# Kernel tuning notes

Measured on AMD Instinct MI355X. Metric: run time of the kernel, lower is better.

The kernel has to match this reference:

```python
import jax, jax.numpy as jnp
import numpy as np

B, L, C, H = 4, 2048, 1024, 16
D = C // H            # head_dim = 64
TAU = 4
SCALE = 1.0 / np.sqrt(D) / TAU  # cos_attn=False path


def setup_inputs() -> dict:
    key = jax.random.key(0)
    ks = jax.random.split(key, 7)
    std = 1.0 / np.sqrt(C)
    return {
        "x": jax.random.normal(ks[0], (B, L, C), dtype=jnp.float32),
        "attn_bias": jax.random.normal(ks[1], (1, 1, L, L), dtype=jnp.float32) * 0.02,
        "W_qkv": jax.random.normal(ks[2], (3 * C, C), dtype=jnp.float32) * std,
        "q_bias": jax.random.normal(ks[3], (C,), dtype=jnp.float32) * 0.02,
        "v_bias": jax.random.normal(ks[4], (C,), dtype=jnp.float32) * 0.02,
        "W_proj": jax.random.normal(ks[5], (C, C), dtype=jnp.float32) * std,
        "b_proj": jax.random.normal(ks[6], (C,), dtype=jnp.float32) * 0.02,
    }


def reference(x, attn_bias, W_qkv, q_bias, v_bias, W_proj, b_proj):
    # qkv projection with bias = cat(q_bias, zeros_k, v_bias)
    bias = jnp.concatenate([q_bias, jnp.zeros_like(q_bias), v_bias])
    qkv = x @ W_qkv.T + bias                      # [B, L, 3C]
    qkv = qkv.reshape(B, L, 3, H, D)
    q, k, v = jnp.moveaxis(qkv, 2, 0)             # each [B, L, H, D]
    q = q.transpose(0, 2, 1, 3)                   # [B, H, L, D]
    k = k.transpose(0, 2, 1, 3)
    v = v.transpose(0, 2, 1, 3)
    # slow_attn: (q*scale) @ k^T + bias -> softmax -> @ v
    scores = jnp.einsum("bhqd,bhkd->bhqk", q * SCALE, k) + attn_bias
    attn = jax.nn.softmax(scores, axis=-1)
    oup = jnp.einsum("bhqk,bhkd->bhqd", attn, v)  # [B, H, L, D]
    oup = oup.transpose(0, 2, 1, 3).reshape(B, L, C)
    return oup @ W_proj.T + b_proj
```

## Files before the change

### kernel.cpp

```cpp
#include <hip/hip_runtime.h>
#include <hip/hip_bf16.h>

typedef unsigned short u16;
typedef unsigned int   u32;

using f32x4  = __attribute__((ext_vector_type(4)))  float;
using f32x16 = __attribute__((ext_vector_type(16))) float;
using s16x8  = __attribute__((ext_vector_type(8)))  short;
using b16x8  = __attribute__((ext_vector_type(8)))  __bf16;
using u32x4  = __attribute__((ext_vector_type(4)))  u32;

#define LOG2E 1.44269504088896f
#define QSC   (0.03125f * LOG2E)

__device__ __forceinline__ f32x4 mfma16(s16x8 a, s16x8 b, f32x4 c) {
  return __builtin_amdgcn_mfma_f32_16x16x32_bf16(
      __builtin_bit_cast(b16x8, a), __builtin_bit_cast(b16x8, b), c, 0, 0, 0);
}
__device__ __forceinline__ f32x16 mfma32(s16x8 a, s16x8 b, f32x16 c) {
  return __builtin_amdgcn_mfma_f32_32x32x16_bf16(
      __builtin_bit_cast(b16x8, a), __builtin_bit_cast(b16x8, b), c, 0, 0, 0);
}

__device__ __forceinline__ u16 f2bf(float f) {
  u32 u = __builtin_bit_cast(u32, f);
  u = (u + 0x7FFFu + ((u >> 16) & 1u)) >> 16;
  return (u16)u;
}
__device__ __forceinline__ float exp2_hw(float x) {
  float r;
  asm("v_exp_f32 %0, %1" : "=v"(r) : "v"(x));
  return r;
}
__device__ __forceinline__ u32 cvtpk(float a, float b) {
  u32 r;
  asm("v_cvt_pk_bf16_f32 %0, %1, %2" : "=v"(r) : "v"(a), "v"(b));
  return r;
}

__device__ __forceinline__ void gload16(const void* g, void* l) {
  __builtin_amdgcn_global_load_lds(
      (const __attribute__((address_space(1))) u32*)g,
      (__attribute__((address_space(3))) u32*)l, 16, 0, 0);
}

__global__ void cvt3(const float* __restrict__ x, const float* __restrict__ wqkv,
                     const float* __restrict__ wproj, u16* __restrict__ out) {
  int i = blockIdx.x * blockDim.x + threadIdx.x;
  const int stride = gridDim.x * blockDim.x;
  for (; i < 3145728; i += stride) {
    const float* src = (i < 2097152) ? x + 4 * (long)i
                     : (i < 2883584) ? wqkv + 4 * ((long)i - 2097152)
                                     : wproj + 4 * ((long)i - 2883584);
    const float4 v = *(const float4*)src;
    ushort4 o;
    o.x = f2bf(v.x); o.y = f2bf(v.y); o.z = f2bf(v.z); o.w = f2bf(v.w);
    ((ushort4*)out)[i] = o;
  }
}

__global__ void bias_rearrange(const float* __restrict__ ab, u16* __restrict__ out) {
  __shared__ u16 T[32][72];
  const int tid  = threadIdx.x;
  const int slot = blockIdx.x >> 5;
  const int kt   = blockIdx.x & 31;

  {
    const int qr = tid >> 3;
    const int fc = (tid & 7) * 8;
    const float* src = ab + (long)(slot * 32 + qr) * 2048 + kt * 64 + fc;
    const float4 a = *(const float4*)(src);
    const float4 b = *(const float4*)(src + 4);
    u16 t[8];
    t[0] = f2bf(a.x * LOG2E); t[1] = f2bf(a.y * LOG2E);
    t[2] = f2bf(a.z * LOG2E); t[3] = f2bf(a.w * LOG2E);
    t[4] = f2bf(b.x * LOG2E); t[5] = f2bf(b.y * LOG2E);
    t[6] = f2bf(b.z * LOG2E); t[7] = f2bf(b.w * LOG2E);
    *(s16x8*)&T[qr][fc] = *(s16x8*)t;
  }
  __syncthreads();

  {
    const int chunk = tid >> 6;
    const int lane  = tid & 63;
    const int q5    = lane & 31;
    const int hi    = lane >> 5;
    u16 o[8];
#pragma unroll
    for (int e = 0; e < 8; ++e) {
      const int vidx = chunk * 8 + e;
      const int kb = vidx >> 4, r = vidx & 15;
      const int key = kb * 32 + (r & 3) + 8 * (r >> 2) + 4 * hi;
      o[e] = T[q5][key];
    }
    *(s16x8*)(out + ((long)blockIdx.x * 256 + tid) * 8) = *(s16x8*)o;
  }
}

template<int EPI>
__global__ __launch_bounds__(256)
void gemm_bt(const u16* __restrict__ A, const u16* __restrict__ Bm,
             int M, int N, int K,
             const float* __restrict__ bias0, const float* __restrict__ bias1,
             u16* __restrict__ oq, u16* __restrict__ ok, u16* __restrict__ ov,
             float* __restrict__ outf)
{
  __shared__ u16 As[2][128 * 32];
  __shared__ u16 Bs[2][128 * 32];

  const int tid  = threadIdx.x;
  const int w    = tid >> 6;
  const int lane = tid & 63;
  const int lr   = lane & 15;
  const int lg   = lane >> 4;
  const int wr   = w >> 1, wc = w & 1;

  const int bm = blockIdx.y, bn = blockIdx.x;

  f32x4 acc[4][4];
#pragma unroll
  for (int i = 0; i < 4; ++i)
#pragma unroll
    for (int j = 0; j < 4; ++j) acc[i][j] = (f32x4){0.f, 0.f, 0.f, 0.f};

  const int rowA = bm * 128 + (tid >> 2);
  const int rowB = bn * 128 + (tid >> 2);
  const int colk = (tid & 3) * 8;

  const u16* ga0 = A  + (long)rowA * K + colk;
  const u16* gb0 = Bm + (long)rowB * K + colk;

  gload16(ga0,          &As[0][w * 512]);
  gload16(ga0 + 64 * K, &As[0][2048 + w * 512]);
  gload16(gb0,          &Bs[0][w * 512]);
  gload16(gb0 + 64 * K, &Bs[0][2048 + w * 512]);
  asm volatile("s_waitcnt vmcnt(0)" ::: "memory");
  __syncthreads();

  const int NT = K >> 5;
  for (int t = 0; t < NT; ++t) {
    const int cur = t & 1;
    if (t + 1 < NT) {
      const u16* ga = ga0 + (t + 1) * 32;
      const u16* gb = gb0 + (t + 1) * 32;
      gload16(ga,          &As[cur ^ 1][w * 512]);
      gload16(ga + 64 * K, &As[cur ^ 1][2048 + w * 512]);
      gload16(gb,          &Bs[cur ^ 1][w * 512]);
      gload16(gb + 64 * K, &Bs[cur ^ 1][2048 + w * 512]);
    }

    s16x8 af[4], bfr[4];
#pragma unroll
    for (int mi = 0; mi < 4; ++mi)
      af[mi] = *(const s16x8*)(&As[cur][(wr * 64 + mi * 16 + lr) * 32 + lg * 8]);
#pragma unroll
    for (int ni = 0; ni < 4; ++ni)
      bfr[ni] = *(const s16x8*)(&Bs[cur][(wc * 64 + ni * 16 + lr) * 32 + lg * 8]);
#pragma unroll
    for (int mi = 0; mi < 4; ++mi)
#pragma unroll
      for (int ni = 0; ni < 4; ++ni)
        acc[mi][ni] = mfma16(af[mi], bfr[ni], acc[mi][ni]);

    asm volatile("s_waitcnt vmcnt(0)" ::: "memory");
    __syncthreads();
  }

  const int gm0 = bm * 128 + wr * 64;
  const int gn0 = bn * 128 + wc * 64;

#pragma unroll
  for (int mi = 0; mi < 4; ++mi) {
#pragma unroll
    for (int ni = 0; ni < 4; ++ni) {
      const int col  = gn0 + ni * 16 + lr;
      const int row0 = gm0 + mi * 16 + lg * 4;
      if (EPI == 0) {
        const int which = col >> 10;
        const int cj    = col & 1023;
        const float badd = (which == 0) ? bias0[cj] : (which == 2 ? bias1[cj] : 0.f);
        const int h = cj >> 6, d = cj & 63;
#pragma unroll
        for (int r = 0; r < 4; ++r) {
          const int rowg = row0 + r;
          const int b = rowg >> 11, l = rowg & 2047;
          const int bh = b * 16 + h;
          float val = acc[mi][ni][r] + badd;
          if (which == 0) val *= QSC;
          const u16 o = f2bf(val);
          if (which == 0)      oq[(bh * 2048 + l) * 64 + d] = o;
          else if (which == 1) ok[(bh * 2048 + l) * 64 + d] = o;
          else {
            const int lp = (l & ~12) | ((l & 4) << 1) | ((l & 8) >> 1);
            ov[(bh * 64 + d) * 2048 + lp] = o;
          }
        }
      } else {
        const float badd = bias0[col];
#pragma unroll
        for (int r = 0; r < 4; ++r)
          outf[(long)(row0 + r) * N + col] = acc[mi][ni][r] + badd;
      }
    }
  }
}

__global__ __launch_bounds__(256)
void flash_attn(const u16* __restrict__ qbuf, const u16* __restrict__ kbuf,
                const u16* __restrict__ vtbuf, const u16* __restrict__ biasr,
                u16* __restrict__ oup)
{
  __shared__ u16 Ks[2][64 * 72];
  __shared__ u16 Vs[2][64 * 72];

  const int tid  = threadIdx.x;
  const int w    = tid >> 6;
  const int lane = tid & 63;
  const int lq   = lane & 31;
  const int hi   = lane >> 5;

  const int bid = blockIdx.x;
  const int swz = (bid & 7) * 128 + (bid >> 3);
  const int bh  = swz >> 4, qt2 = swz & 15;
  const long base = (long)bh * (2048 * 64);

  const int qrow = qt2 * 128 + w * 32 + lq;
  s16x8 qf[4];
  {
    const u16* qp = qbuf + base + qrow * 64 + 8 * hi;
#pragma unroll
    for (int s = 0; s < 4; ++s) qf[s] = *(const s16x8*)(qp + 16 * s);
  }

  f32x16 oacc0, oacc1;
  float lacc[8];
#pragma unroll
  for (int r = 0; r < 16; ++r) { oacc0[r] = 0.f; oacc1[r] = 0.f; }
#pragma unroll
  for (int r = 0; r < 8; ++r) lacc[r] = 0.f;

  const u16* bslice = biasr + (long)(qt2 * 4 + w) * 65536 + lane * 8;

  const int sr  = tid >> 3;
  const int scc = tid & 7;
  const u16* kg = kbuf  + base + sr * 64   + scc * 8;
  const u16* vg = vtbuf + base + sr * 2048 + scc * 8;
  const int wo0 = sr * 72 + scc * 8;
  const int wo1 = (32 + sr) * 72 + scc * 8;

  {
    const s16x8 a0 = *(const s16x8*)(kg);
    const s16x8 a1 = *(const s16x8*)(kg + 2048);
    const s16x8 b0 = *(const s16x8*)(vg);
    const s16x8 b1 = *(const s16x8*)(vg + 65536);
    *(s16x8*)(&Ks[0][wo0]) = a0;  *(s16x8*)(&Ks[0][wo1]) = a1;
    *(s16x8*)(&Vs[0][wo0]) = b0;  *(s16x8*)(&Vs[0][wo1]) = b1;
  }
  __syncthreads();

  for (int kt = 0; kt < 32; ++kt) {
    const int cur = kt & 1;

    s16x8 nk0, nk1, nv0, nv1;
    if (kt < 31) {
      const u16* kn = kg + (kt + 1) * 4096;
      const u16* vn = vg + (kt + 1) * 64;
      nk0 = *(const s16x8*)(kn);
      nk1 = *(const s16x8*)(kn + 2048);
      nv0 = *(const s16x8*)(vn);
      nv1 = *(const s16x8*)(vn + 65536);
    }

    s16x8 kf0[4], kf1[4], vf0[4], vf1[4];
    {
      const u16* kb0 = &Ks[cur][lq * 72];
      const u16* kb1 = &Ks[cur][(32 + lq) * 72];
      const u16* vb0 = &Vs[cur][lq * 72];
      const u16* vb1 = &Vs[cur][(32 + lq) * 72];
#pragma unroll
      for (int s = 0; s < 4; ++s) {
        const int off = (2 * s + hi) * 8;
        kf0[s] = *(const s16x8*)(kb0 + off);
        kf1[s] = *(const s16x8*)(kb1 + off);
        vf0[s] = *(const s16x8*)(vb0 + off);
        vf1[s] = *(const s16x8*)(vb1 + off);
      }
    }

    u32x4 bb[4];
#pragma unroll
    for (int k = 0; k < 4; ++k)
      bb[k] = *(const u32x4*)(bslice + kt * 2048 + k * 512);

    f32x16 sa0, sa1;
#pragma unroll
    for (int jw = 0; jw < 8; ++jw) {
      const u32 w0 = bb[jw >> 2][jw & 3];
      const u32 w1 = bb[2 + (jw >> 2)][jw & 3];
      sa0[2 * jw]     = __builtin_bit_cast(float, w0 << 16);
      sa0[2 * jw + 1] = __builtin_bit_cast(float, w0 & 0xFFFF0000u);
      sa1[2 * jw]     = __builtin_bit_cast(float, w1 << 16);
      sa1[2 * jw + 1] = __builtin_bit_cast(float, w1 & 0xFFFF0000u);
    }

#pragma unroll
    for (int s = 0; s < 4; ++s) sa0 = mfma32(kf0[s], qf[s], sa0);
#pragma unroll
    for (int s = 0; s < 4; ++s) sa1 = mfma32(kf1[s], qf[s], sa1);

#pragma unroll
    for (int r = 0; r < 16; ++r) {
      sa0[r] = exp2_hw(sa0[r]);
      sa1[r] = exp2_hw(sa1[r]);
    }
#pragma unroll
    for (int r = 0; r < 8; ++r)
      lacc[r] += (sa0[r] + sa0[r + 8]) + (sa1[r] + sa1[r + 8]);

    s16x8 pf[4];
#pragma unroll
    for (int ks = 0; ks < 4; ++ks) {
      const f32x16 ps = (ks & 2) ? sa1 : sa0;
      const int o = (ks & 1) * 8;
      u32x4 tt;
      tt[0] = cvtpk(ps[o + 0], ps[o + 1]);
      tt[1] = cvtpk(ps[o + 2], ps[o + 3]);
      tt[2] = cvtpk(ps[o + 4], ps[o + 5]);
      tt[3] = cvtpk(ps[o + 6], ps[o + 7]);
      pf[ks] = __builtin_bit_cast(s16x8, tt);
    }

#pragma unroll
    for (int ks = 0; ks < 4; ++ks) {
      oacc0 = mfma32(vf0[ks], pf[ks], oacc0);
      oacc1 = mfma32(vf1[ks], pf[ks], oacc1);
    }

    if (kt < 31) {
      *(s16x8*)(&Ks[cur ^ 1][wo0]) = nk0;
      *(s16x8*)(&Ks[cur ^ 1][wo1]) = nk1;
      *(s16x8*)(&Vs[cur ^ 1][wo0]) = nv0;
      *(s16x8*)(&Vs[cur ^ 1][wo1]) = nv1;
    }
    __syncthreads();
  }

  u32 (*Os)[32][33] = (u32(*)[32][33])&Ks[0][0];
  const int b = bh >> 4, h = bh & 15;
  float l = ((lacc[0] + lacc[1]) + (lacc[2] + lacc[3]))
          + ((lacc[4] + lacc[5]) + (lacc[6] + lacc[7]));
  l += __shfl_xor(l, 32, 64);
  const float inv = 1.f / l;
#pragma unroll
  for (int i = 0; i < 8; ++i) {
    const int idx = (i & 1) + 2 * hi + 4 * (i >> 1);
    Os[w][lq][idx]      = cvtpk(oacc0[2 * i] * inv, oacc0[2 * i + 1] * inv);
    Os[w][lq][idx + 16] = cvtpk(oacc1[2 * i] * inv, oacc1[2 * i + 1] * inv);
  }
  __syncthreads();
#pragma unroll
  for (int it = 0; it < 4; ++it) {
    const int q = it * 8 + (lane >> 3);
    const int c = (lane & 7) * 4;
    u32x4 v;
#pragma unroll
    for (int j = 0; j < 4; ++j) v[j] = Os[w][q][c + j];
    const long row = (long)(b * 2048 + qt2 * 128 + w * 32 + q);
    *(u32x4*)(oup + row * 1024 + h * 64 + (lane & 7) * 8) = v;
  }
}

extern "C" void kernel_launch(void* const* d_in, const int* in_sizes, int n_in,
                              void* d_out, int out_size, void* d_ws, size_t ws_size,
                              hipStream_t stream) {
  const float* x     = (const float*)d_in[0];
  const float* ab    = (const float*)d_in[1];
  const float* wqkv  = (const float*)d_in[2];
  const float* qbias = (const float*)d_in[3];
  const float* vbias = (const float*)d_in[4];
  const float* wproj = (const float*)d_in[5];
  const float* bproj = (const float*)d_in[6];
  float* out = (float*)d_out;

  char* ws = (char*)d_ws;
  if (ws_size < 83886080u) return;
  u16* xb     = (u16*)(ws);
  u16* wqkvb  = (u16*)(ws + 16777216);
  u16* wprojb = (u16*)(ws + 23068672);
  u16* biasr  = (u16*)(ws + 25165824);
  u16* qbuf   = (u16*)(ws + 33554432);
  u16* kbuf   = (u16*)(ws + 50331648);
  u16* vtbuf  = (u16*)(ws + 67108864);

  cvt3<<<dim3(2048), dim3(256), 0, stream>>>(x, wqkv, wproj, xb);
  bias_rearrange<<<dim3(2048), dim3(256), 0, stream>>>(ab, biasr);

  gemm_bt<0><<<dim3(24, 64), dim3(256), 0, stream>>>(
      xb, wqkvb, 8192, 3072, 1024, qbias, vbias, qbuf, kbuf, vtbuf, nullptr);

  flash_attn<<<dim3(1024), dim3(256), 0, stream>>>(qbuf, kbuf, vtbuf, biasr, xb);

  gemm_bt<1><<<dim3(8, 64), dim3(256), 0, stream>>>(
      xb, wprojb, 8192, 1024, 1024, bproj, nullptr, nullptr, nullptr, nullptr, out);
}
```

Measured before the change: 229.8 us.

## Triple-buffer GEMM shared-memory tiles with partial vmcnt waits

Moves the bf16 GEMM from double to triple buffering of the A/B shared tiles. Loads for tile t+2 are issued right after a single barrier per iteration, and a partial vmcnt wait lets the following tile's loads stay in flight while the current tile is computed. This removes one full vmcnt(0) drain and one barrier per k-step, in exchange for 50% more LDS per block, which may reduce occupancy. It relies on gload16 being a direct-to-LDS load counted by vmcnt, so that vmcnt(4) exactly matches the four loads of one stage.

```diff
diff --git a/kernel.cpp b/kernel.cpp
--- a/kernel.cpp
+++ b/kernel.cpp
@@ -105,8 +105,8 @@
              u16* __restrict__ oq, u16* __restrict__ ok, u16* __restrict__ ov,
              float* __restrict__ outf)
 {
-  __shared__ u16 As[2][128 * 32];
-  __shared__ u16 Bs[2][128 * 32];
+  __shared__ u16 As[3][128 * 32];
+  __shared__ u16 Bs[3][128 * 32];
 
   const int tid  = threadIdx.x;
   const int w    = tid >> 6;
@@ -130,24 +130,26 @@
   const u16* ga0 = A  + (long)rowA * K + colk;
   const u16* gb0 = Bm + (long)rowB * K + colk;
 
-  gload16(ga0,          &As[0][w * 512]);
-  gload16(ga0 + 64 * K, &As[0][2048 + w * 512]);
-  gload16(gb0,          &Bs[0][w * 512]);
-  gload16(gb0 + 64 * K, &Bs[0][2048 + w * 512]);
-  asm volatile("s_waitcnt vmcnt(0)" ::: "memory");
-  __syncthreads();
+#define GSTAGE(BUF, T)                                          \
+  {                                                             \
+    const u16* ga = ga0 + (T) * 32;                             \
+    const u16* gb = gb0 + (T) * 32;                             \
+    gload16(ga,          &As[BUF][w * 512]);                    \
+    gload16(ga + 64 * K, &As[BUF][2048 + w * 512]);             \
+    gload16(gb,          &Bs[BUF][w * 512]);                    \
+    gload16(gb + 64 * K, &Bs[BUF][2048 + w * 512]);             \
+  }
+
+  GSTAGE(0, 0);
+  GSTAGE(1, 1);
 
   const int NT = K >> 5;
+  int cur = 0, nx2 = 2;
   for (int t = 0; t < NT; ++t) {
-    const int cur = t & 1;
-    if (t + 1 < NT) {
-      const u16* ga = ga0 + (t + 1) * 32;
-      const u16* gb = gb0 + (t + 1) * 32;
-      gload16(ga,          &As[cur ^ 1][w * 512]);
-      gload16(ga + 64 * K, &As[cur ^ 1][2048 + w * 512]);
-      gload16(gb,          &Bs[cur ^ 1][w * 512]);
-      gload16(gb + 64 * K, &Bs[cur ^ 1][2048 + w * 512]);
-    }
+    if (t + 1 < NT) asm volatile("s_waitcnt vmcnt(4)" ::: "memory");
+    else            asm volatile("s_waitcnt vmcnt(0)" ::: "memory");
+    __builtin_amdgcn_s_barrier();
+    if (t + 2 < NT) GSTAGE(nx2, t + 2);
 
     s16x8 af[4], bfr[4];
 #pragma unroll
@@ -162,9 +164,10 @@
       for (int ni = 0; ni < 4; ++ni)
         acc[mi][ni] = mfma16(af[mi], bfr[ni], acc[mi][ni]);
 
-    asm volatile("s_waitcnt vmcnt(0)" ::: "memory");
-    __syncthreads();
-  }
+    cur = (cur == 2) ? 0 : cur + 1;
+    nx2 = (nx2 == 2) ? 0 : nx2 + 1;
+  }
+#undef GSTAGE
 
   const int gm0 = bm * 128 + wr * 64;
   const int gn0 = bn * 128 + wc * 64;
```

Result: no change. 230.5 us (+0.3%).
